# Performance work log

Measured on AMD Instinct MI355X. Metric: run time of the kernel, lower is better.

Reference implementation:

```python
import jax, jax.numpy as jnp
import numpy as np
from jax import lax

B, CEN, CDE, H, W = 4, 256, 256, 64, 64   # de is (B,CDE,H,W); en is (B,CEN,2H,2W)
EMB, K, SCALE = 64, 5, 2
DN = ('NCHW', 'OIHW', 'NCHW')


def conv2d(x, w, b=None, pad=0):
    y = lax.conv_general_dilated(x, w, (1, 1), [(pad, pad), (pad, pad)], dimension_numbers=DN)
    return y if b is None else y + b[None, :, None, None]


def up2(x):
    # F.interpolate(scale_factor=2) default mode='nearest'
    return jnp.repeat(jnp.repeat(x, 2, axis=2), 2, axis=3)


def carafe(de, kernels, k, scale):
    # de: (B,C,H,W); kernels: (B,k*k,H*scale,W*scale), softmax-normalized over dim 1
    b, c, h, w = de.shape
    pad = k // 2
    dep = jnp.pad(de, ((0, 0), (0, 0), (pad, pad), (pad, pad)))
    # (B, C, k*k, H, W): all k*k shifted views of de (zero-padded borders)
    patches = jnp.stack([dep[:, :, dy:dy + h, dx:dx + w]
                         for dy in range(k) for dx in range(k)], axis=2)
    # each output pixel (i,j) reuses the window at source (i//scale, j//scale)
    ker = kernels.reshape(b, k * k, h, scale, w, scale)
    out = jnp.einsum('bkhxwy,bckhw->bchxwy', ker, patches)
    return out.reshape(b, c, h * scale, w * scale)


def xavier_uniform(key, shape):
    fan_out = shape[0] * shape[2] * shape[3]
    fan_in = shape[1] * shape[2] * shape[3]
    limit = float(np.sqrt(6.0 / (fan_in + fan_out)))
    return jax.random.uniform(key, shape, jnp.float32, -limit, limit)


def setup_inputs() -> dict:
    key = jax.random.key(0)
    ks = jax.random.split(key, 7)
    return {
        'en': jax.random.normal(ks[0], (B, CEN, 2 * H, 2 * W), jnp.float32),
        'de': jax.random.normal(ks[1], (B, CDE, H, W), jnp.float32),
        'w_gate': xavier_uniform(ks[2], (1, CDE, 1, 1)),
        'b_gate': jnp.zeros((1,), jnp.float32),
        'w_cen': xavier_uniform(ks[3], (EMB, CEN, 1, 1)),
        'b_cen': jnp.zeros((EMB,), jnp.float32),
        'w_cde': xavier_uniform(ks[4], (EMB, CDE, 1, 1)),
        'w_ce': xavier_uniform(ks[5], (K * K, EMB, 3, 3)),
        'b_ce': jnp.zeros((K * K,), jnp.float32),
    }


def reference(en, de, w_gate, b_gate, w_cen, b_cen, w_cde, w_ce, b_ce):
    # GateGenerator: sigmoid(interpolate(conv1x1(de), x2))
    gate = jax.nn.sigmoid(up2(conv2d(de, w_gate, b_gate)))
    # SemiShift: shared 3x3 content encoder on compressed en and upsampled compressed de
    enc = conv2d(en, w_cen, b_cen)
    dec = conv2d(de, w_cde)          # no bias
    logits = conv2d(enc, w_ce, b_ce, pad=1) + up2(conv2d(dec, w_ce, b_ce, pad=1))
    kernels = jax.nn.softmax(logits, axis=1)
    return gate * en + (1.0 - gate) * carafe(de, kernels, K, SCALE)
```

## Files before the change

### kernel.cpp

```cpp
#include <hip/hip_runtime.h>
#include <math.h>

#define BB 4
#define C 256
#define H 64
#define W 64
#define HW 4096
#define HO 128
#define WO 128
#define HWO 16384
#define EMB 64

typedef __bf16 bf16x8 __attribute__((ext_vector_type(8)));
typedef __bf16 bf16x4 __attribute__((ext_vector_type(4)));
typedef float  f32x4  __attribute__((ext_vector_type(4)));

__device__ __forceinline__ f32x4 mfma16(bf16x8 a, bf16x8 b, f32x4 c) {
    return __builtin_amdgcn_mfma_f32_16x16x32_bf16(a, b, c, 0, 0, 0);
}

__global__ void k_prep2(const float* __restrict__ w_cen,
                        const float* __restrict__ w_cde,
                        const float* __restrict__ w_gate,
                        const float* __restrict__ w_ce,
                        __bf16* __restrict__ wbf_cen,
                        __bf16* __restrict__ wdec5,
                        __bf16* __restrict__ w3) {
    for (int idx = blockIdx.x * blockDim.x + threadIdx.x; idx < 16384;
         idx += gridDim.x * blockDim.x)
        wbf_cen[idx] = (__bf16)w_cen[idx];
    for (int idx = blockIdx.x * blockDim.x + threadIdx.x; idx < 20480;
         idx += gridDim.x * blockDim.x) {
        int c = idx & 255, m = (idx >> 8) & 15;
        float v;
        if (idx < 16384) v = w_cde[idx];
        else             v = (m == 0) ? w_gate[c] : 0.f;
        wdec5[idx] = (__bf16)v;
    }
    for (int idx = blockIdx.x * blockDim.x + threadIdx.x; idx < 18432;
         idx += gridDim.x * blockDim.x) {
        int e = idx & 63;
        int m = (idx >> 6) & 15;
        int mt = (idx >> 10) & 1;
        int tap = idx >> 11;
        int q = mt * 16 + m;
        int dy = tap / 3, dx = tap % 3;
        w3[idx] = (q < 25) ? (__bf16)w_ce[((q * EMB + e) * 3 + dy) * 3 + dx]
                           : (__bf16)0.0f;
    }
}

__global__ __launch_bounds__(256) void k_gemm1(
        const float* __restrict__ en, const float* __restrict__ de,
        const __bf16* __restrict__ wbf_cen, const __bf16* __restrict__ wdec5,
        const float* __restrict__ b_cen, const float* __restrict__ b_gate,
        __bf16* __restrict__ enc_t, __bf16* __restrict__ dec_t,
        float* __restrict__ gate_lr) {
    __shared__ float xs[32 * 64];
    int t = threadIdx.x;
    int w = t >> 6, lane = t & 63;
    int n = lane & 15, q = lane >> 4;
    bool isenc = blockIdx.x < 1024;
    const float* X; const __bf16* Wt; __bf16* Y; int plane, px0, b;
    if (isenc) {
        int blk = blockIdx.x; b = blk >> 8; px0 = (blk & 255) << 6;
        X = en + (size_t)b * C * HWO; plane = HWO; Wt = wbf_cen;
        Y = enc_t + (size_t)b * HWO * EMB;
    } else {
        int blk = blockIdx.x - 1024; b = blk >> 6; px0 = (blk & 63) << 6;
        X = de + (size_t)b * C * HW; plane = HW; Wt = wdec5;
        Y = dec_t + (size_t)b * HW * EMB;
    }
    int px = w * 16 + n;
    f32x4 acc[5] = {};
    for (int kc = 0; kc < 8; kc++) {
        int c0 = kc * 32;
        __syncthreads();
        #pragma unroll
        for (int i = 0; i < 2; i++) {
            int idx = i * 256 + t;
            int c = idx >> 4, p4 = (idx & 15) << 2;
            float4 v = *(const float4*)(X + (size_t)(c0 + c) * plane + px0 + p4);
            *(float4*)(xs + c * 64 + p4) = v;
        }
        __syncthreads();
        bf16x8 af[5];
        #pragma unroll
        for (int mt = 0; mt < 4; mt++)
            af[mt] = *(const bf16x8*)(Wt + (mt * 16 + n) * C + c0 + q * 8);
        if (!isenc)
            af[4] = *(const bf16x8*)(Wt + (64 + n) * C + c0 + q * 8);
        bf16x8 bv;
        #pragma unroll
        for (int j = 0; j < 8; j++)
            bv[j] = (__bf16)xs[(q * 8 + j) * 64 + px];
        #pragma unroll
        for (int mt = 0; mt < 4; mt++)
            acc[mt] = mfma16(af[mt], bv, acc[mt]);
        if (!isenc)
            acc[4] = mfma16(af[4], bv, acc[4]);
    }
    int gpx = px0 + px;
    #pragma unroll
    for (int mt = 0; mt < 4; mt++) {
        int e0 = mt * 16 + q * 4;
        bf16x4 ov;
        #pragma unroll
        for (int r = 0; r < 4; r++) {
            float bias = isenc ? b_cen[e0 + r] : 0.f;
            ov[r] = (__bf16)(acc[mt][r] + bias);
        }
        *(bf16x4*)(Y + (size_t)gpx * EMB + e0) = ov;
    }
    if (!isenc && q == 0)
        gate_lr[b * HW + gpx] = 1.f / (1.f + __expf(-(acc[4][0] + b_gate[0])));
}

__global__ __launch_bounds__(256) void k_conv3m(
        const __bf16* __restrict__ enc_t, const __bf16* __restrict__ dec_t,
        const __bf16* __restrict__ w3, const float* __restrict__ b_ce,
        float* __restrict__ tmp1, float* __restrict__ tmp2) {
    __shared__ __bf16 sfr[8 * 3 * 66 * 8];
    int t = threadIdx.x;
    int w = t >> 6, lane = t & 63;
    int n = lane & 15, q = lane >> 4;
    bool hi = blockIdx.x < 1024;
    const __bf16* src; float* dst; int b, y, width, plane, x0;
    if (hi) {
        int blk = blockIdx.x; b = blk >> 8; int r = blk & 255;
        y = r >> 1; x0 = (r & 1) * 64;
        width = WO; plane = HWO;
        src = enc_t + (size_t)b * HWO * EMB; dst = tmp1;
    } else {
        int blk = blockIdx.x - 1024; b = blk >> 6; y = blk & 63; x0 = 0;
        width = W; plane = HW;
        src = dec_t + (size_t)b * HW * EMB; dst = tmp2;
    }
    bf16x8 zf;
    #pragma unroll
    for (int j = 0; j < 8; j++) zf[j] = (__bf16)0.0f;
    for (int idx = t; idx < 1584; idx += 256) {
        int f = idx & 7;
        int rem = idx >> 3;
        int xloc = rem % 66, row = rem / 66;
        int yy = y + row - 1, xg = x0 - 1 + xloc;
        bf16x8 v = zf;
        if ((unsigned)yy < (unsigned)width && (unsigned)xg < (unsigned)width)
            v = *(const bf16x8*)(src + ((size_t)yy * width + xg) * EMB + f * 8);
        *(bf16x8*)(sfr + (((f * 3) + row) * 66 + xloc) * 8) = v;
    }
    __syncthreads();

    int x = w * 16 + n;
    f32x4 acc[2] = {};
    #pragma unroll
    for (int row = 0; row < 3; row++) {
        #pragma unroll
        for (int dx = 0; dx < 3; dx++) {
            int tap = row * 3 + dx;
            #pragma unroll
            for (int kc = 0; kc < 2; kc++) {
                bf16x8 bv = *(const bf16x8*)(
                    sfr + ((((kc * 4 + q) * 3) + row) * 66 + x + dx) * 8);
                #pragma unroll
                for (int mt = 0; mt < 2; mt++) {
                    bf16x8 av = *(const bf16x8*)(
                        w3 + ((tap * 2 + mt) * 16 + n) * EMB + kc * 32 + q * 8);
                    acc[mt] = mfma16(av, bv, acc[mt]);
                }
            }
        }
    }
    #pragma unroll
    for (int mt = 0; mt < 2; mt++) {
        #pragma unroll
        for (int r = 0; r < 4; r++) {
            int m = mt * 16 + q * 4 + r;
            if (m < 25)
                dst[((size_t)(b * 25 + m)) * plane + y * width + x0 + x] =
                    acc[mt][r] + b_ce[m];
        }
    }
}

__global__ __launch_bounds__(256) void k_softmax(
        const float* __restrict__ tmp1, const float* __restrict__ tmp2,
        float* __restrict__ kbuf) {
    __shared__ float red[4][64];
    int t = threadIdx.x;
    int tx = t & 63, qg = t >> 6;
    int gp = blockIdx.x * 64 + tx;
    int b = gp >> 14, p = gp & 16383;
    int i = p >> 7, j = p & 127;
    int pl = (i >> 1) * W + (j >> 1);
    int q0 = qg * 7;
    int nq = (qg < 3) ? 7 : 4;
    float l[7];
    float mx = -1e30f;
    for (int iq = 0; iq < nq; iq++) {
        int qq = q0 + iq;
        l[iq] = tmp1[((size_t)(b * 25 + qq) << 14) + p]
              + tmp2[((size_t)(b * 25 + qq) << 12) + pl];
        mx = fmaxf(mx, l[iq]);
    }
    red[qg][tx] = mx;
    __syncthreads();
    mx = fmaxf(fmaxf(red[0][tx], red[1][tx]), fmaxf(red[2][tx], red[3][tx]));
    float s = 0.f;
    for (int iq = 0; iq < nq; iq++) { l[iq] = __expf(l[iq] - mx); s += l[iq]; }
    __syncthreads();
    red[qg][tx] = s;
    __syncthreads();
    s = red[0][tx] + red[1][tx] + red[2][tx] + red[3][tx];
    float inv = 1.f / s;
    float* kb = kbuf + (size_t)gp * 28;
    for (int iq = 0; iq < nq; iq++) kb[q0 + iq] = l[iq] * inv;
    if (qg == 3) { kb[25] = 0.f; kb[26] = 0.f; kb[27] = 0.f; }
}

__global__ __launch_bounds__(256) void k_final(
        const float* __restrict__ en, const float* __restrict__ de,
        const float* __restrict__ kbuf, const float* __restrict__ gate_lr,
        float* __restrict__ out) {
    __shared__ float sde[16][20][21];
    int t = threadIdx.x;
    int tlx = blockIdx.x & 3, tly = blockIdx.x >> 2;
    int c0 = blockIdx.y * 16;
    int b = blockIdx.z;
    int y0 = tly * 16, x0 = tlx * 16;

    const float* dbase = de + ((size_t)b * C + c0) * HW;
    for (int idx = t; idx < 16 * 400; idx += 256) {
        int c = idx / 400, rem = idx % 400;
        int yy0 = rem / 20, xx0 = rem % 20;
        int yy = y0 - 2 + yy0, xx = x0 - 2 + xx0;
        float v = 0.f;
        if ((unsigned)yy < (unsigned)H && (unsigned)xx < (unsigned)W)
            v = dbase[(size_t)c * HW + yy * W + xx];
        sde[c][yy0][xx0] = v;
    }

    int ty = t >> 4, tx = t & 15;
    int yl = y0 + ty, xl = x0 + tx;
    float4 kf[4][7];
    #pragma unroll
    for (int hp = 0; hp < 4; hp++) {
        int ii = 2 * yl + (hp >> 1), jj = 2 * xl + (hp & 1);
        const float4* kb = (const float4*)(
            kbuf + ((size_t)b * HWO + ii * WO + jj) * 28);
        #pragma unroll
        for (int v = 0; v < 7; v++) kf[hp][v] = kb[v];
    }
    float g = gate_lr[b * HW + yl * W + xl];
    float gm = 1.f - g;
    __syncthreads();

    const float* ebase = en + ((size_t)b * C + c0) * HWO;
    float* obase = out + ((size_t)b * C + c0) * HWO;
    for (int c = 0; c < 16; c++) {
        float acc0 = 0.f, acc1 = 0.f, acc2 = 0.f, acc3 = 0.f;
        #pragma unroll
        for (int dy = 0; dy < 5; dy++) {
            #pragma unroll
            for (int dx = 0; dx < 5; dx++) {
                float v = sde[c][ty + dy][tx + dx];
                int k = dy * 5 + dx;
                acc0 += ((const float*)&kf[0][0])[k] * v;
                acc1 += ((const float*)&kf[1][0])[k] * v;
                acc2 += ((const float*)&kf[2][0])[k] * v;
                acc3 += ((const float*)&kf[3][0])[k] * v;
            }
        }
        size_t cc = (size_t)c * HWO;
        float2 e0 = *(const float2*)(ebase + cc + (2 * yl) * WO + 2 * xl);
        float2 e1 = *(const float2*)(ebase + cc + (2 * yl + 1) * WO + 2 * xl);
        float2 o0, o1;
        o0.x = g * e0.x + gm * acc0;  o0.y = g * e0.y + gm * acc1;
        o1.x = g * e1.x + gm * acc2;  o1.y = g * e1.y + gm * acc3;
        *(float2*)(obase + cc + (2 * yl) * WO + 2 * xl) = o0;
        *(float2*)(obase + cc + (2 * yl + 1) * WO + 2 * xl) = o1;
    }
}

extern "C" void kernel_launch(void* const* d_in, const int* in_sizes, int n_in,
                              void* d_out, int out_size, void* d_ws, size_t ws_size,
                              hipStream_t stream) {
    const float* en     = (const float*)d_in[0];
    const float* de     = (const float*)d_in[1];
    const float* w_gate = (const float*)d_in[2];
    const float* b_gate = (const float*)d_in[3];
    const float* w_cen  = (const float*)d_in[4];
    const float* b_cen  = (const float*)d_in[5];
    const float* w_cde  = (const float*)d_in[6];
    const float* w_ce   = (const float*)d_in[7];
    const float* b_ce   = (const float*)d_in[8];
    float* out = (float*)d_out;

    __bf16* wsb     = (__bf16*)d_ws;
    __bf16* wbf_cen = wsb;
    __bf16* wdec5   = wbf_cen + 16384;
    __bf16* w3      = wdec5 + 20480;
    __bf16* enc_t   = w3 + 18432;
    __bf16* dec_t   = enc_t + 4194304;
    float* wsf     = (float*)((char*)d_ws + (size_t)(16384 + 20480 + 18432
                              + 4194304 + 1048576) * 2);
    float* tmp1    = wsf;
    float* tmp2    = tmp1 + 1638400;
    float* gate_lr = tmp2 + 409600;
    float* kbuf    = gate_lr + 16384;

    k_prep2<<<80, 256, 0, stream>>>(w_cen, w_cde, w_gate, w_ce,
                                    wbf_cen, wdec5, w3);
    k_gemm1<<<1280, 256, 0, stream>>>(en, de, wbf_cen, wdec5, b_cen, b_gate,
                                      enc_t, dec_t, gate_lr);
    k_conv3m<<<1280, 256, 0, stream>>>(enc_t, dec_t, w3, b_ce, tmp1, tmp2);
    k_softmax<<<1024, 256, 0, stream>>>(tmp1, tmp2, kbuf);
    k_final<<<dim3(16, 16, 4), 256, 0, stream>>>(en, de, kbuf, gate_lr, out);
}
```

Baseline: 241.1 us.

## Double-buffer GEMM1 loads with larger pixel tiles and reshape CARAFE final tile

k_gemm1 now handles 128 pixels per block with two N-tiles per wave. Its shared-memory staging is double-buffered, so the global loads for the next channel chunk are issued while MFMAs run on the current one, and one barrier is removed per iteration. k_final switches from 16x16 to 32x8 low-res tiles, which gives wider contiguous rows for the en/out accesses and a smaller halo overhead. It also loads only 25 kernel weights instead of 28. In exchange, register and shared-memory use per block rise and the gemm grid is halved, which can lower occupancy.

```diff
diff --git a/kernel.cpp b/kernel.cpp
--- a/kernel.cpp
+++ b/kernel.cpp
@@ -56,64 +56,92 @@
         const float* __restrict__ b_cen, const float* __restrict__ b_gate,
         __bf16* __restrict__ enc_t, __bf16* __restrict__ dec_t,
         float* __restrict__ gate_lr) {
-    __shared__ float xs[32 * 64];
+    __shared__ float xs[2][32][136];
     int t = threadIdx.x;
     int w = t >> 6, lane = t & 63;
     int n = lane & 15, q = lane >> 4;
-    bool isenc = blockIdx.x < 1024;
+    bool isenc = blockIdx.x < 512;
     const float* X; const __bf16* Wt; __bf16* Y; int plane, px0, b;
     if (isenc) {
-        int blk = blockIdx.x; b = blk >> 8; px0 = (blk & 255) << 6;
+        int blk = blockIdx.x; b = blk >> 7; px0 = (blk & 127) << 7;
         X = en + (size_t)b * C * HWO; plane = HWO; Wt = wbf_cen;
         Y = enc_t + (size_t)b * HWO * EMB;
     } else {
-        int blk = blockIdx.x - 1024; b = blk >> 6; px0 = (blk & 63) << 6;
+        int blk = blockIdx.x - 512; b = blk >> 5; px0 = (blk & 31) << 7;
         X = de + (size_t)b * C * HW; plane = HW; Wt = wdec5;
         Y = dec_t + (size_t)b * HW * EMB;
     }
-    int px = w * 16 + n;
-    f32x4 acc[5] = {};
+    int scc = t >> 5;
+    int sp4 = (t & 31) << 2;
+    float4 pre[4];
+    #pragma unroll
+    for (int i = 0; i < 4; i++)
+        pre[i] = *(const float4*)(X + (size_t)(i * 8 + scc) * plane + px0 + sp4);
+    #pragma unroll
+    for (int i = 0; i < 4; i++)
+        *(float4*)(&xs[0][i * 8 + scc][sp4]) = pre[i];
+    __syncthreads();
+
+    f32x4 acc[4][2] = {};
+    f32x4 accg[2] = {};
     for (int kc = 0; kc < 8; kc++) {
+        int cur = kc & 1;
+        if (kc < 7) {
+            int c1 = (kc + 1) * 32;
+            #pragma unroll
+            for (int i = 0; i < 4; i++)
+                pre[i] = *(const float4*)(X + (size_t)(c1 + i * 8 + scc) * plane
+                                          + px0 + sp4);
+        }
         int c0 = kc * 32;
+        bf16x8 af[4];
+        #pragma unroll
+        for (int mt = 0; mt < 4; mt++)
+            af[mt] = *(const bf16x8*)(Wt + (size_t)(mt * 16 + n) * C + c0 + q * 8);
+        bf16x8 bv[2];
+        #pragma unroll
+        for (int nt = 0; nt < 2; nt++) {
+            int px = w * 32 + nt * 16 + n;
+            #pragma unroll
+            for (int j = 0; j < 8; j++)
+                bv[nt][j] = (__bf16)xs[cur][q * 8 + j][px];
+        }
+        #pragma unroll
+        for (int mt = 0; mt < 4; mt++) {
+            acc[mt][0] = mfma16(af[mt], bv[0], acc[mt][0]);
+            acc[mt][1] = mfma16(af[mt], bv[1], acc[mt][1]);
+        }
+        if (!isenc) {
+            bf16x8 ag = *(const bf16x8*)(Wt + (size_t)(64 + n) * C + c0 + q * 8);
+            accg[0] = mfma16(ag, bv[0], accg[0]);
+            accg[1] = mfma16(ag, bv[1], accg[1]);
+        }
+        if (kc < 7) {
+            #pragma unroll
+            for (int i = 0; i < 4; i++)
+                *(float4*)(&xs[cur ^ 1][i * 8 + scc][sp4]) = pre[i];
+        }
         __syncthreads();
-        #pragma unroll
-        for (int i = 0; i < 2; i++) {
-            int idx = i * 256 + t;
-            int c = idx >> 4, p4 = (idx & 15) << 2;
-            float4 v = *(const float4*)(X + (size_t)(c0 + c) * plane + px0 + p4);
-            *(float4*)(xs + c * 64 + p4) = v;
-        }
-        __syncthreads();
-        bf16x8 af[5];
-        #pragma unroll
-        for (int mt = 0; mt < 4; mt++)
-            af[mt] = *(const bf16x8*)(Wt + (mt * 16 + n) * C + c0 + q * 8);
-        if (!isenc)
-            af[4] = *(const bf16x8*)(Wt + (64 + n) * C + c0 + q * 8);
-        bf16x8 bv;
-        #pragma unroll
-        for (int j = 0; j < 8; j++)
-            bv[j] = (__bf16)xs[(q * 8 + j) * 64 + px];
-        #pragma unroll
-        for (int mt = 0; mt < 4; mt++)
-            acc[mt] = mfma16(af[mt], bv, acc[mt]);
-        if (!isenc)
-            acc[4] = mfma16(af[4], bv, acc[4]);
-    }
-    int gpx = px0 + px;
-    #pragma unroll
-    for (int mt = 0; mt < 4; mt++) {
-        int e0 = mt * 16 + q * 4;
-        bf16x4 ov;
-        #pragma unroll
-        for (int r = 0; r < 4; r++) {
-            float bias = isenc ? b_cen[e0 + r] : 0.f;
-            ov[r] = (__bf16)(acc[mt][r] + bias);
-        }
-        *(bf16x4*)(Y + (size_t)gpx * EMB + e0) = ov;
-    }
-    if (!isenc && q == 0)
-        gate_lr[b * HW + gpx] = 1.f / (1.f + __expf(-(acc[4][0] + b_gate[0])));
+    }
+
+    #pragma unroll
+    for (int nt = 0; nt < 2; nt++) {
+        int gpx = px0 + w * 32 + nt * 16 + n;
+        #pragma unroll
+        for (int mt = 0; mt < 4; mt++) {
+            int e0 = mt * 16 + q * 4;
+            bf16x4 ov;
+            #pragma unroll
+            for (int r = 0; r < 4; r++) {
+                float bias = isenc ? b_cen[e0 + r] : 0.f;
+                ov[r] = (__bf16)(acc[mt][nt][r] + bias);
+            }
+            *(bf16x4*)(Y + (size_t)gpx * EMB + e0) = ov;
+        }
+        if (!isenc && q == 0)
+            gate_lr[b * HW + gpx] =
+                1.f / (1.f + __expf(-(accg[nt][0] + b_gate[0])));
+    }
 }
 
 __global__ __launch_bounds__(256) void k_conv3m(
@@ -218,67 +246,69 @@
     if (qg == 3) { kb[25] = 0.f; kb[26] = 0.f; kb[27] = 0.f; }
 }
 
+#define NCH 16
 __global__ __launch_bounds__(256) void k_final(
         const float* __restrict__ en, const float* __restrict__ de,
         const float* __restrict__ kbuf, const float* __restrict__ gate_lr,
         float* __restrict__ out) {
-    __shared__ float sde[16][20][21];
+    __shared__ float sde[NCH][12][36];
     int t = threadIdx.x;
-    int tlx = blockIdx.x & 3, tly = blockIdx.x >> 2;
-    int c0 = blockIdx.y * 16;
+    int x0 = (blockIdx.x & 1) * 32, y0 = (blockIdx.x >> 1) * 8;
+    int c0 = blockIdx.y * NCH;
     int b = blockIdx.z;
-    int y0 = tly * 16, x0 = tlx * 16;
 
     const float* dbase = de + ((size_t)b * C + c0) * HW;
-    for (int idx = t; idx < 16 * 400; idx += 256) {
-        int c = idx / 400, rem = idx % 400;
-        int yy0 = rem / 20, xx0 = rem % 20;
-        int yy = y0 - 2 + yy0, xx = x0 - 2 + xx0;
+    for (int idx = t; idx < NCH * 432; idx += 256) {
+        int c = idx / 432, rem = idx % 432;
+        int row = rem / 36, col = rem % 36;
+        int yy = y0 - 2 + row, xx = x0 - 2 + col;
         float v = 0.f;
         if ((unsigned)yy < (unsigned)H && (unsigned)xx < (unsigned)W)
             v = dbase[(size_t)c * HW + yy * W + xx];
-        sde[c][yy0][xx0] = v;
-    }
-
-    int ty = t >> 4, tx = t & 15;
+        sde[c][row][col] = v;
+    }
+
+    int tx = t & 31, ty = t >> 5;
     int yl = y0 + ty, xl = x0 + tx;
-    float4 kf[4][7];
+    float kern[4][25];
     #pragma unroll
     for (int hp = 0; hp < 4; hp++) {
         int ii = 2 * yl + (hp >> 1), jj = 2 * xl + (hp & 1);
-        const float4* kb = (const float4*)(
-            kbuf + ((size_t)b * HWO + ii * WO + jj) * 28);
-        #pragma unroll
-        for (int v = 0; v < 7; v++) kf[hp][v] = kb[v];
+        const float* kb = kbuf + ((size_t)b * HWO + ii * WO + jj) * 28;
+        #pragma unroll
+        for (int v = 0; v < 6; v++)
+            *(float4*)&kern[hp][v * 4] = *(const float4*)(kb + v * 4);
+        kern[hp][24] = kb[24];
     }
     float g = gate_lr[b * HW + yl * W + xl];
     float gm = 1.f - g;
     __syncthreads();
 
-    const float* ebase = en + ((size_t)b * C + c0) * HWO;
-    float* obase = out + ((size_t)b * C + c0) * HWO;
-    for (int c = 0; c < 16; c++) {
-        float acc0 = 0.f, acc1 = 0.f, acc2 = 0.f, acc3 = 0.f;
+    const float* ebase = en + ((size_t)b * C + c0) * HWO + (2 * yl) * WO + 2 * xl;
+    float* obase = out + ((size_t)b * C + c0) * HWO + (2 * yl) * WO + 2 * xl;
+    #pragma unroll 2
+    for (int c = 0; c < NCH; c++) {
+        float a0 = 0.f, a1 = 0.f, a2 = 0.f, a3 = 0.f;
         #pragma unroll
         for (int dy = 0; dy < 5; dy++) {
             #pragma unroll
             for (int dx = 0; dx < 5; dx++) {
                 float v = sde[c][ty + dy][tx + dx];
                 int k = dy * 5 + dx;
-                acc0 += ((const float*)&kf[0][0])[k] * v;
-                acc1 += ((const float*)&kf[1][0])[k] * v;
-                acc2 += ((const float*)&kf[2][0])[k] * v;
-                acc3 += ((const float*)&kf[3][0])[k] * v;
+                a0 += kern[0][k] * v;
+                a1 += kern[1][k] * v;
+                a2 += kern[2][k] * v;
+                a3 += kern[3][k] * v;
             }
         }
         size_t cc = (size_t)c * HWO;
-        float2 e0 = *(const float2*)(ebase + cc + (2 * yl) * WO + 2 * xl);
-        float2 e1 = *(const float2*)(ebase + cc + (2 * yl + 1) * WO + 2 * xl);
+        float2 e0 = *(const float2*)(ebase + cc);
+        float2 e1 = *(const float2*)(ebase + cc + WO);
         float2 o0, o1;
-        o0.x = g * e0.x + gm * acc0;  o0.y = g * e0.y + gm * acc1;
-        o1.x = g * e1.x + gm * acc2;  o1.y = g * e1.y + gm * acc3;
-        *(float2*)(obase + cc + (2 * yl) * WO + 2 * xl) = o0;
-        *(float2*)(obase + cc + (2 * yl + 1) * WO + 2 * xl) = o1;
+        o0.x = g * e0.x + gm * a0;  o0.y = g * e0.y + gm * a1;
+        o1.x = g * e1.x + gm * a2;  o1.y = g * e1.y + gm * a3;
+        *(float2*)(obase + cc) = o0;
+        *(float2*)(obase + cc + WO) = o1;
     }
 }
 
@@ -311,8 +341,8 @@
 
     k_prep2<<<80, 256, 0, stream>>>(w_cen, w_cde, w_gate, w_ce,
                                     wbf_cen, wdec5, w3);
-    k_gemm1<<<1280, 256, 0, stream>>>(en, de, wbf_cen, wdec5, b_cen, b_gate,
-                                      enc_t, dec_t, gate_lr);
+    k_gemm1<<<640, 256, 0, stream>>>(en, de, wbf_cen, wdec5, b_cen, b_gate,
+                                     enc_t, dec_t, gate_lr);
     k_conv3m<<<1280, 256, 0, stream>>>(enc_t, dec_t, w3, b_ce, tmp1, tmp2);
     k_softmax<<<1024, 256, 0, stream>>>(tmp1, tmp2, kbuf);
     k_final<<<dim3(16, 16, 4), 256, 0, stream>>>(en, de, kbuf, gate_lr, out);
```

Measured after the change: 234.8 us. -2.6%, faster.
